# Performance work log

Hardware: AMD Instinct MI355X
Metric: run time of the kernel (lower is better)

## Reference

```python
import jax, jax.numpy as jnp
import numpy as np

MAX_NEIGHBORS = 10
D = 1024
N = 16384

def setup_inputs() -> dict:
    key = jax.random.key(0)
    ks = jax.random.split(key, 12)
    s = 0.05
    inp = {
        'target_embedding': jax.random.normal(ks[0], (D,), jnp.float32),
        'all_embeddings': jax.random.normal(ks[1], (N, D), jnp.float32),
        'similarity_matrix': jax.random.normal(ks[2], (N, N), jnp.float32),
        # attention_net: Linear(2D->D), ReLU, Linear(D->1)
        'W_att1': jax.random.normal(ks[3], (2 * D, D), jnp.float32) * s,
        'b_att1': jnp.zeros((D,), jnp.float32),
        'W_att2': jax.random.normal(ks[4], (D, 1), jnp.float32) * s,
        'b_att2': jnp.zeros((1,), jnp.float32),
        # neighbor_count_net: Linear(D->D//2), ReLU, Linear(D//2->1), Sigmoid
        'W_cnt1': jax.random.normal(ks[5], (D, D // 2), jnp.float32) * s,
        'b_cnt1': jnp.zeros((D // 2,), jnp.float32),
        'W_cnt2': jax.random.normal(ks[6], (D // 2, 1), jnp.float32) * s,
        'b_cnt2': jnp.zeros((1,), jnp.float32),
        'target_idx': 123,
    }
    return inp

def reference(target_embedding, all_embeddings, similarity_matrix,
              W_att1, b_att1, W_att2, b_att2,
              W_cnt1, b_cnt1, W_cnt2, b_cnt2, target_idx):
    # dynamic neighbor count: int(sigmoid(mlp(x)) * max_neighbors), clamped to [1, max_neighbors]
    h = jax.nn.relu(target_embedding @ W_cnt1 + b_cnt1)
    frac = jax.nn.sigmoid(h @ W_cnt2 + b_cnt2)[0]
    dynamic_k = jnp.clip(jnp.floor(frac * MAX_NEIGHBORS).astype(jnp.int32), 1, MAX_NEIGHBORS)

    # top-(K+1) over the target's similarity row; statically sized, mask to dynamic_k
    row = similarity_matrix[target_idx]
    _, top_idx = jax.lax.top_k(row, MAX_NEIGHBORS + 1)  # [K+1]
    # stable compaction: move target_idx (if present) to the end, keep order otherwise
    order = jnp.where(top_idx == target_idx, MAX_NEIGHBORS + 1, jnp.arange(MAX_NEIGHBORS + 1))
    neighbor_idx = top_idx[jnp.argsort(order)][:MAX_NEIGHBORS]  # [K]
    valid = jnp.arange(MAX_NEIGHBORS) < dynamic_k              # [K]

    neighbor_emb = all_embeddings[neighbor_idx]                 # [K, D]
    target_exp = jnp.broadcast_to(target_embedding, (MAX_NEIGHBORS, D))
    pair = jnp.concatenate([target_exp, neighbor_emb], axis=-1)  # [K, 2D]
    scores = (jax.nn.relu(pair @ W_att1 + b_att1) @ W_att2 + b_att2)[:, 0]  # [K]
    scores = jnp.where(valid, scores, -jnp.inf)
    weights = jax.nn.softmax(scores)                            # zeros at invalid slots
    aggregated = weights @ neighbor_emb                         # [D]
    return aggregated, weights, neighbor_idx, weights
```

## Files before the change

kernel.cpp:

```cpp
#include <hip/hip_runtime.h>
#include <math.h>

#define NN 16384
#define DD 1024
#define HD 512

#define WS_DK  0
#define WS_CTR 2
#define WS_NB  4
#define WS_UV  32
#define WS_HP  11296

__global__ void __launch_bounds__(256) k1(const float* __restrict__ x,
                                          const float* __restrict__ Wc1,
                                          const float* __restrict__ sim,
                                          const int* __restrict__ tidx,
                                          float* __restrict__ ws,
                                          float* __restrict__ out) {
    const int t = threadIdx.x;
    const int b = blockIdx.x;
    const int lane = t & 63, wave = t >> 6;

    if (b < 32) {
        __shared__ float xs[32];
        const int ibase = b * 32;
        if (t < 32) xs[t] = x[ibase + t];
        __syncthreads();
        #pragma unroll
        for (int jj = 0; jj < 2; ++jj) {
            const int j = t + jj * 256;
            float acc = 0.f;
            const float* W = Wc1 + (size_t)ibase * HD + j;
            #pragma unroll 8
            for (int ii = 0; ii < 32; ++ii) acc += xs[ii] * W[(size_t)ii * HD];
            ws[WS_HP + b * HD + j] = acc;
        }
        return;
    }
    if (b == 32) {
        for (int i = t; i < 11 * DD; i += 256) ws[WS_UV + i] = 0.f;
        if (t == 0) ((int*)ws)[WS_CTR] = 0;
        return;
    }

    const int tgt = tidx[0];
    const float4* row4 = (const float4*)(sim + (size_t)tgt * NN);
    float vals[64];
    #pragma unroll
    for (int c = 0; c < 16; ++c) {
        float4 v = row4[c * 256 + t];
        vals[c * 4 + 0] = v.x; vals[c * 4 + 1] = v.y;
        vals[c * 4 + 2] = v.z; vals[c * 4 + 3] = v.w;
    }
    float bv = -INFINITY; int bs = 0;
    #pragma unroll
    for (int s = 0; s < 64; ++s) if (vals[s] > bv) { bv = vals[s]; bs = s; }

    __shared__ float wvs[4];
    __shared__ int   wgs[4];
    __shared__ int   winner;
    __shared__ int   toplist[11];

    for (int it = 0; it < 11; ++it) {
        float cv = bv;
        int   cg = (bs >> 2) * 1024 + t * 4 + (bs & 3);
        for (int off = 32; off > 0; off >>= 1) {
            float ov = __shfl_down(cv, off);
            int   og = __shfl_down(cg, off);
            if (ov > cv || (ov == cv && og < cg)) { cv = ov; cg = og; }
        }
        if (lane == 0) { wvs[wave] = cv; wgs[wave] = cg; }
        __syncthreads();
        if (t == 0) {
            float fv = wvs[0]; int fg = wgs[0];
            for (int w = 1; w < 4; ++w)
                if (wvs[w] > fv || (wvs[w] == fv && wgs[w] < fg)) { fv = wvs[w]; fg = wgs[w]; }
            toplist[it] = fg;
            winner = fg;
        }
        __syncthreads();
        const int w = winner;
        if (((w >> 2) & 255) == t) {
            vals[((w >> 10) << 2) | (w & 3)] = -INFINITY;
            bv = -INFINITY; bs = 0;
            #pragma unroll
            for (int s = 0; s < 64; ++s) if (vals[s] > bv) { bv = vals[s]; bs = s; }
        }
    }
    if (t == 0) {
        int cnt = 0;
        int* nbp = (int*)ws + WS_NB;
        for (int i = 0; i < 11 && cnt < 10; ++i) {
            int v = toplist[i];
            if (v != tgt) { nbp[cnt] = v; out[1034 + cnt] = (float)v; ++cnt; }
        }
    }
}

__global__ void __launch_bounds__(256) k2(const float* __restrict__ x,
                                          const float* __restrict__ emb,
                                          const float* __restrict__ W1,
                                          const float* __restrict__ ba1,
                                          const float* __restrict__ W2,
                                          const float* __restrict__ ba2,
                                          const float* __restrict__ bc1,
                                          const float* __restrict__ Wc2,
                                          const float* __restrict__ bc2,
                                          float* __restrict__ ws,
                                          float* __restrict__ out) {
    const int t = threadIdx.x;
    const int b = blockIdx.x;
    const int lane = t & 63, wave = t >> 6;

    __shared__ float xs[32];
    __shared__ float es[10][32];
    __shared__ int   nb[10];
    __shared__ float red[256];
    __shared__ float sc[10];
    __shared__ float wl[10];
    __shared__ int   lastFlag;

    if (b < 128) {
        const int jc = b & 3, ic = b >> 2;
        const int ibase = ic * 32;
        const int j = jc * 256 + t;
        if (t < 10) nb[t] = ((const int*)ws)[WS_NB + t];
        if (t < 32) xs[t] = x[ibase + t];
        __syncthreads();
        for (int idx = t; idx < 320; idx += 256) {
            int k = idx >> 5, ii = idx & 31;
            es[k][ii] = emb[(size_t)nb[k] * DD + ibase + ii];
        }
        __syncthreads();
        float acc[11];
        #pragma unroll
        for (int k = 0; k < 11; ++k) acc[k] = 0.f;
        const float* Wt = W1 + (size_t)ibase * DD + j;
        const float* Wb = W1 + (size_t)(1024 + ibase) * DD + j;
        for (int ii = 0; ii < 32; ++ii) {
            float wt = Wt[(size_t)ii * DD];
            float wb = Wb[(size_t)ii * DD];
            acc[10] += xs[ii] * wt;
            #pragma unroll
            for (int k = 0; k < 10; ++k) acc[k] += es[k][ii] * wb;
        }
        #pragma unroll
        for (int k = 0; k < 11; ++k) atomicAdd(&ws[WS_UV + k * DD + j], acc[k]);
    } else {
        float acc = 0.f;
        #pragma unroll
        for (int jj = 0; jj < 2; ++jj) {
            int j = t + jj * 256;
            float s = 0.f;
            #pragma unroll 8
            for (int c = 0; c < 32; ++c) s += ws[WS_HP + c * HD + j];
            float h = fmaxf(s + bc1[j], 0.f);
            acc += h * Wc2[j];
        }
        red[t] = acc;
        __syncthreads();
        for (int off = 128; off > 0; off >>= 1) {
            if (t < off) red[t] += red[t + off];
            __syncthreads();
        }
        if (t == 0) {
            float z = red[0] + bc2[0];
            float frac = 1.f / (1.f + expf(-z));
            int dk = (int)floorf(frac * 10.f);
            ((int*)ws)[WS_DK] = dk < 1 ? 1 : (dk > 10 ? 10 : dk);
        }
    }

    __syncthreads();
    __threadfence();
    if (t == 0) lastFlag = (atomicAdd((int*)ws + WS_CTR, 1) == 128);
    __syncthreads();
    if (!lastFlag) return;
    __threadfence();

    if (t < 10) nb[t] = ((const int*)ws)[WS_NB + t];
    __syncthreads();
    for (int k = wave; k < 10; k += 4) {
        float acc = 0.f;
        #pragma unroll
        for (int m = 0; m < 16; ++m) {
            int j = lane + m * 64;
            float h = ws[WS_UV + 10 * DD + j] + ws[WS_UV + k * DD + j] + ba1[j];
            acc += fmaxf(h, 0.f) * W2[j];
        }
        #pragma unroll
        for (int off = 32; off > 0; off >>= 1) acc += __shfl_down(acc, off);
        if (lane == 0) sc[k] = acc + ba2[0];
    }
    __syncthreads();
    if (t == 0) {
        int dk = ((const int*)ws)[WS_DK];
        float v[10];
        float m = -INFINITY;
        for (int k = 0; k < 10; ++k) {
            v[k] = (k < dk) ? sc[k] : -INFINITY;
            if (v[k] > m) m = v[k];
        }
        float sum = 0.f;
        for (int k = 0; k < 10; ++k) { v[k] = expf(v[k] - m); sum += v[k]; }
        for (int k = 0; k < 10; ++k) wl[k] = v[k] / sum;
    }
    __syncthreads();
    #pragma unroll
    for (int jj = 0; jj < 4; ++jj) {
        int j = t + jj * 256;
        float a = 0.f;
        #pragma unroll
        for (int k = 0; k < 10; ++k) a += wl[k] * emb[(size_t)nb[k] * DD + j];
        out[j] = a;
    }
    if (t < 10) { out[1024 + t] = wl[t]; out[1044 + t] = wl[t]; }
}

extern "C" void kernel_launch(void* const* d_in, const int* in_sizes, int n_in,
                              void* d_out, int out_size, void* d_ws, size_t ws_size,
                              hipStream_t stream) {
    const float* x    = (const float*)d_in[0];
    const float* emb  = (const float*)d_in[1];
    const float* sim  = (const float*)d_in[2];
    const float* W1   = (const float*)d_in[3];
    const float* ba1  = (const float*)d_in[4];
    const float* W2   = (const float*)d_in[5];
    const float* ba2  = (const float*)d_in[6];
    const float* Wc1  = (const float*)d_in[7];
    const float* bc1  = (const float*)d_in[8];
    const float* Wc2  = (const float*)d_in[9];
    const float* bc2  = (const float*)d_in[10];
    const int*   tidx = (const int*)d_in[11];
    float* out = (float*)d_out;
    float* ws  = (float*)d_ws;

    hipLaunchKernelGGL(k1, dim3(34),  dim3(256), 0, stream, x, Wc1, sim, tidx, ws, out);
    hipLaunchKernelGGL(k2, dim3(129), dim3(256), 0, stream,
                       x, emb, W1, ba1, W2, ba2, bc1, Wc2, bc2, ws, out);
}
```

Measured before the change: 44.77 us.

## Fuse attention score reduction into k2 column blocks with in-block K-split reduction

Reworks k2 so each of 32 blocks owns 32 output columns of the first attention layer and splits the 2048-long input dimension across 8 thread groups. The partial sums are reduced in shared memory, then ReLU and the W2 dot are applied in-block, and only 10 partial scores per block are atomically added to workspace. This replaces 11K global atomics and the last-block rescan of hidden vectors, and shrinks the workspace zeroing in k1. The cost is fewer blocks (33 instead of 129), so less parallelism for streaming the 8MB W1 matrix, plus explicit __threadfence calls removed in favour of atomics.

```diff
diff --git a/kernel.cpp b/kernel.cpp
--- a/kernel.cpp
+++ b/kernel.cpp
@@ -8,8 +8,8 @@
 #define WS_DK  0
 #define WS_CTR 2
 #define WS_NB  4
-#define WS_UV  32
-#define WS_HP  11296
+#define WS_SC  16
+#define WS_HP  64
 
 __global__ void __launch_bounds__(256) k1(const float* __restrict__ x,
                                           const float* __restrict__ Wc1,
@@ -38,7 +38,7 @@
         return;
     }
     if (b == 32) {
-        for (int i = t; i < 11 * DD; i += 256) ws[WS_UV + i] = 0.f;
+        if (t < 10) ws[WS_SC + t] = 0.f;
         if (t == 0) ((int*)ws)[WS_CTR] = 0;
         return;
     }
@@ -110,43 +110,87 @@
                                           float* __restrict__ out) {
     const int t = threadIdx.x;
     const int b = blockIdx.x;
-    const int lane = t & 63, wave = t >> 6;
-
-    __shared__ float xs[32];
-    __shared__ float es[10][32];
-    __shared__ int   nb[10];
-    __shared__ float red[256];
-    __shared__ float sc[10];
-    __shared__ float wl[10];
-    __shared__ int   lastFlag;
-
-    if (b < 128) {
-        const int jc = b & 3, ic = b >> 2;
-        const int ibase = ic * 32;
-        const int j = jc * 256 + t;
+
+    __shared__ int    nb[10];
+    __shared__ float4 xs4[256];
+    __shared__ float4 es4[10][256];
+    __shared__ float  red[8][32][13];
+    __shared__ float  wl[10];
+    __shared__ int    shlast;
+
+    if (b < 32) {
+        const int jl  = t & 31;
+        const int seg = t >> 5;
+        const int jg  = b * 32 + jl;
         if (t < 10) nb[t] = ((const int*)ws)[WS_NB + t];
-        if (t < 32) xs[t] = x[ibase + t];
-        __syncthreads();
-        for (int idx = t; idx < 320; idx += 256) {
-            int k = idx >> 5, ii = idx & 31;
-            es[k][ii] = emb[(size_t)nb[k] * DD + ibase + ii];
-        }
-        __syncthreads();
+        __syncthreads();
+        xs4[t] = ((const float4*)x)[t];
+        #pragma unroll
+        for (int r = 0; r < 10; ++r)
+            es4[r][t] = ((const float4*)(emb + (size_t)nb[r] * DD))[t];
+        __syncthreads();
+
         float acc[11];
         #pragma unroll
         for (int k = 0; k < 11; ++k) acc[k] = 0.f;
-        const float* Wt = W1 + (size_t)ibase * DD + j;
-        const float* Wb = W1 + (size_t)(1024 + ibase) * DD + j;
-        for (int ii = 0; ii < 32; ++ii) {
-            float wt = Wt[(size_t)ii * DD];
-            float wb = Wb[(size_t)ii * DD];
-            acc[10] += xs[ii] * wt;
-            #pragma unroll
-            for (int k = 0; k < 10; ++k) acc[k] += es[k][ii] * wb;
-        }
-        #pragma unroll
-        for (int k = 0; k < 11; ++k) atomicAdd(&ws[WS_UV + k * DD + j], acc[k]);
+        const int i0 = seg * 128;
+        const int c0 = i0 >> 2;
+        const float* Wt = W1 + (size_t)i0 * DD + jg;
+        const float* Wb = W1 + (size_t)(1024 + i0) * DD + jg;
+        for (int c = 0; c < 32; ++c) {
+            float4 xv = xs4[c0 + c];
+            float4 ev[10];
+            #pragma unroll
+            for (int k = 0; k < 10; ++k) ev[k] = es4[k][c0 + c];
+            #pragma unroll
+            for (int q = 0; q < 4; ++q) {
+                const size_t off = (size_t)(c * 4 + q) * DD;
+                const float wt = Wt[off];
+                const float wb = Wb[off];
+                acc[10] += reinterpret_cast<const float*>(&xv)[q] * wt;
+                #pragma unroll
+                for (int k = 0; k < 10; ++k)
+                    acc[k] += reinterpret_cast<const float*>(&ev[k])[q] * wb;
+            }
+        }
+        #pragma unroll
+        for (int k = 0; k < 11; ++k) red[seg][jl][k] = acc[k];
+        __syncthreads();
+
+        float psc[10];
+        #pragma unroll
+        for (int k = 0; k < 10; ++k) psc[k] = 0.f;
+        if (t < 32) {
+            float v[11];
+            #pragma unroll
+            for (int k = 0; k < 11; ++k) {
+                float s = 0.f;
+                #pragma unroll
+                for (int g = 0; g < 8; ++g) s += red[g][t][k];
+                v[k] = s;
+            }
+            const float bj = ba1[b * 32 + t];
+            const float w2 = W2[b * 32 + t];
+            #pragma unroll
+            for (int k = 0; k < 10; ++k)
+                psc[k] = fmaxf(v[10] + v[k] + bj, 0.f) * w2;
+        }
+        if (t < 64) {
+            #pragma unroll
+            for (int k = 0; k < 10; ++k) {
+                float s = psc[k];
+                for (int off = 32; off > 0; off >>= 1) s += __shfl_down(s, off);
+                psc[k] = s;
+            }
+        }
+        if (t == 0) {
+            float dep = 0.f;
+            #pragma unroll
+            for (int k = 0; k < 10; ++k) dep += atomicAdd(&ws[WS_SC + k], psc[k]);
+            asm volatile("" :: "v"(dep));
+        }
     } else {
+        float* redc = (float*)red;
         float acc = 0.f;
         #pragma unroll
         for (int jj = 0; jj < 2; ++jj) {
@@ -157,53 +201,40 @@
             float h = fmaxf(s + bc1[j], 0.f);
             acc += h * Wc2[j];
         }
-        red[t] = acc;
+        redc[t] = acc;
         __syncthreads();
         for (int off = 128; off > 0; off >>= 1) {
-            if (t < off) red[t] += red[t + off];
+            if (t < off) redc[t] += redc[t + off];
             __syncthreads();
         }
         if (t == 0) {
-            float z = red[0] + bc2[0];
+            float z = redc[0] + bc2[0];
             float frac = 1.f / (1.f + expf(-z));
             int dk = (int)floorf(frac * 10.f);
-            ((int*)ws)[WS_DK] = dk < 1 ? 1 : (dk > 10 ? 10 : dk);
+            dk = dk < 1 ? 1 : (dk > 10 ? 10 : dk);
+            int old = atomicExch((int*)ws + WS_DK, dk);
+            asm volatile("" :: "v"(old));
         }
     }
 
     __syncthreads();
-    __threadfence();
-    if (t == 0) lastFlag = (atomicAdd((int*)ws + WS_CTR, 1) == 128);
+    if (t == 0) shlast = (atomicAdd((int*)ws + WS_CTR, 1) == 32);
     __syncthreads();
-    if (!lastFlag) return;
-    __threadfence();
+    if (!shlast) return;
 
     if (t < 10) nb[t] = ((const int*)ws)[WS_NB + t];
-    __syncthreads();
-    for (int k = wave; k < 10; k += 4) {
-        float acc = 0.f;
-        #pragma unroll
-        for (int m = 0; m < 16; ++m) {
-            int j = lane + m * 64;
-            float h = ws[WS_UV + 10 * DD + j] + ws[WS_UV + k * DD + j] + ba1[j];
-            acc += fmaxf(h, 0.f) * W2[j];
-        }
-        #pragma unroll
-        for (int off = 32; off > 0; off >>= 1) acc += __shfl_down(acc, off);
-        if (lane == 0) sc[k] = acc + ba2[0];
-    }
-    __syncthreads();
     if (t == 0) {
-        int dk = ((const int*)ws)[WS_DK];
-        float v[10];
+        int dk = atomicAdd((int*)ws + WS_DK, 0);
+        float sv[10];
         float m = -INFINITY;
         for (int k = 0; k < 10; ++k) {
-            v[k] = (k < dk) ? sc[k] : -INFINITY;
-            if (v[k] > m) m = v[k];
+            float s = atomicAdd(&ws[WS_SC + k], 0.f) + ba2[0];
+            sv[k] = (k < dk) ? s : -INFINITY;
+            if (sv[k] > m) m = sv[k];
         }
         float sum = 0.f;
-        for (int k = 0; k < 10; ++k) { v[k] = expf(v[k] - m); sum += v[k]; }
-        for (int k = 0; k < 10; ++k) wl[k] = v[k] / sum;
+        for (int k = 0; k < 10; ++k) { sv[k] = expf(sv[k] - m); sum += sv[k]; }
+        for (int k = 0; k < 10; ++k) wl[k] = sv[k] / sum;
     }
     __syncthreads();
     #pragma unroll
@@ -235,7 +266,7 @@
     float* out = (float*)d_out;
     float* ws  = (float*)d_ws;
 
-    hipLaunchKernelGGL(k1, dim3(34),  dim3(256), 0, stream, x, Wc1, sim, tidx, ws, out);
-    hipLaunchKernelGGL(k2, dim3(129), dim3(256), 0, stream,
+    hipLaunchKernelGGL(k1, dim3(34), dim3(256), 0, stream, x, Wc1, sim, tidx, ws, out);
+    hipLaunchKernelGGL(k2, dim3(33), dim3(256), 0, stream,
                        x, emb, W1, ba1, W2, ba2, bc1, Wc2, bc2, ws, out);
 }
```

Measured after the change: 49.00 us. 1.09x slower.
